# Performance work log

Measured on AMD Instinct MI355X. Metric: run time of the kernel, lower is better.

## Reference

```python
import jax, jax.numpy as jnp
import numpy as np

N_TIME, N_BATCH, N_STATE, N_FORCE = 64, 8192, 32, 16
DT = 0.05          # implicit (backward-Euler) step size
NEWTON_ITERS = 6   # fixed Newton-Raphson iteration count (converges well below fp32 eps here)


def setup_inputs() -> dict:
    key = jax.random.key(0)
    k = jax.random.split(key, 5)
    return {
        "y0": jax.random.normal(k[0], (N_BATCH, N_STATE), jnp.float32) * 0.1,
        "forces": jax.random.normal(k[1], (N_TIME, N_BATCH, N_FORCE), jnp.float32),
        "W": jax.random.normal(k[2], (N_STATE, N_STATE), jnp.float32) / np.float32(np.sqrt(N_STATE)),
        "U": jax.random.normal(k[3], (N_STATE, N_FORCE), jnp.float32) / np.float32(np.sqrt(N_FORCE)),
        "b": jax.random.normal(k[4], (N_STATE,), jnp.float32) * 0.01,
        "n": N_TIME,
    }


def reference(y0, forces, W, U, b, n):
    """Sequential recursive nonlinear solve, block_size=1, ZeroPredictor guess.

    Each step solves R(y_k) = y_k - y_{k-1} - dt*tanh(W y_k + U u_k + b) = 0
    via Newton-Raphson with a batched dense solve of the diagonal Jacobian
    block J[1] = I - dt*diag(1-t^2) W (the Thomas factorization for a single
    step reduces to this dense solve).
    """
    S = y0.shape[-1]
    I = jnp.eye(S, dtype=y0.dtype)

    def step(y_prev, u):
        fu = u @ U.T + b                      # [B,S] constant per Newton solve
        y = jnp.zeros_like(y_prev)            # ZeroPredictor initial guess
        for _ in range(NEWTON_ITERS):         # plain Newton-Raphson
            t = jnp.tanh(y @ W.T + fu)        # [B,S]
            R = y - y_prev - DT * t           # residual [B,S]
            J = I - DT * ((1.0 - t * t)[..., :, None] * W)  # [B,S,S] dR/dy
            y = y - jnp.linalg.solve(J, R[..., None])[..., 0]
        return y, y

    _, ys = jax.lax.scan(step, y0, forces[1:n])   # sequential recursion over time
    return jnp.concatenate([y0[None], ys], axis=0)  # result[0] = y0
```

## Files before the change

### kernel.cpp

```cpp
#include <hip/hip_runtime.h>

#define NT 64
#define NB 8192
#define NS 32
#define NF 16
#define DT 0.05f

typedef float f32x2 __attribute__((ext_vector_type(2)));
typedef float f32x4 __attribute__((ext_vector_type(4)));

__device__ __forceinline__ f32x2 tanh2(f32x2 x) {
    const float K = 2.8853900817779268f;
    float e0 = __builtin_amdgcn_exp2f(K * x[0]);
    float e1 = __builtin_amdgcn_exp2f(K * x[1]);
    float r0 = __builtin_amdgcn_rcpf(e0 + 1.0f);
    float r1 = __builtin_amdgcn_rcpf(e1 + 1.0f);
    f32x2 r;
    r[0] = fmaf(-2.0f, r0, 1.0f);
    r[1] = fmaf(-2.0f, r1, 1.0f);
    return r;
}

__global__ __launch_bounds__(256, 2) void rnes_kernel(
    const float* __restrict__ y0,
    const float* __restrict__ forces,
    const float* __restrict__ W,
    const float* __restrict__ U,
    const float* __restrict__ bias,
    float* __restrict__ out)
{
    const int lane = threadIdx.x & 63;
    const int wv   = threadIdx.x >> 6;
    const int b    = lane >> 4;
    const int p    = lane & 15;
    const int batch = blockIdx.x * 16 + wv * 4 + b;

    const int got = __builtin_amdgcn_update_dpp(0, p, 0x121, 0xF, 0xF, true) & 15;
    const int dir = (got == ((p + 1) & 15)) ? 1 : 15;

    f32x2 WA[16], WB[16];
#pragma unroll
    for (int j = 0; j < 16; ++j) {
        const int q = (p + dir * j) & 15;
        WA[j] = *(const f32x2*)(W + (2*p)   * NS + 2*q);
        WB[j] = *(const f32x2*)(W + (2*p+1) * NS + 2*q);
    }
#pragma unroll
    for (int j = 0; j < 16; ++j)
        asm volatile("" : "+v"(WA[j]), "+v"(WB[j]));

    f32x2 UA[8], UB[8];
#pragma unroll
    for (int f = 0; f < 8; ++f) {
        UA[f] = *(const f32x2*)(U + (2*p)   * NF + 2*f);
        UB[f] = *(const f32x2*)(U + (2*p+1) * NF + 2*f);
    }
#pragma unroll
    for (int f = 0; f < 8; ++f)
        asm volatile("" : "+v"(UA[f]), "+v"(UB[f]));

    const f32x2 b2 = *(const f32x2*)(bias + 2*p);

    f32x2 yp = *(const f32x2*)(y0 + (size_t)batch * NS + 2*p);
    __builtin_nontemporal_store(yp, (f32x2*)(out + (size_t)batch * NS + 2*p));
    f32x2 ypp = yp;

    const size_t fstep = (size_t)NB * NF;
    const f32x4* fb = (const f32x4*)(forces + (size_t)batch * NF);
    f32x4 upf[4];
#pragma unroll
    for (int j = 0; j < 4; ++j)
        upf[j] = __builtin_nontemporal_load(&fb[(fstep >> 2) + j]);

    for (int k = 1; k < NT; ++k) {
        f32x2 sA = (f32x2){0.f, 0.f}, sB = (f32x2){0.f, 0.f};
#pragma unroll
        for (int f = 0; f < 8; ++f) {
            f32x4 u4 = upf[f >> 1];
            f32x2 u2 = (f & 1) ? (f32x2){u4[2], u4[3]} : (f32x2){u4[0], u4[1]};
            sA = UA[f] * u2 + sA;
            sB = UB[f] * u2 + sB;
        }
        const float fu0 = b2[0] + sA[0] + sA[1];
        const float fu1 = b2[1] + sB[0] + sB[1];

        {
            int kn = (k + 1 < NT) ? (k + 1) : (NT - 1);
#pragma unroll
            for (int j = 0; j < 4; ++j)
                upf[j] = __builtin_nontemporal_load(&fb[(size_t)kn * (fstep >> 2) + j]);
        }

        f32x2 y;
        y[0] = yp[0] + (yp[0] - ypp[0]);
        y[1] = yp[1] + (yp[1] - ypp[1]);

        auto iterate = [&]() {
            const int y0i = __float_as_int(y[0]);
            const int y1i = __float_as_int(y[1]);
            f32x2 accA = (f32x2){fu0, 0.f};
            f32x2 accB = (f32x2){fu1, 0.f};
            accA = WA[0] * y + accA;
            accB = WB[0] * y + accB;
#define RNES_HOP(J)                                                            \
            {                                                                  \
                f32x2 yq;                                                      \
                yq[0] = __int_as_float(__builtin_amdgcn_update_dpp(            \
                    0, y0i, 0x120 + (J), 0xF, 0xF, true));                     \
                yq[1] = __int_as_float(__builtin_amdgcn_update_dpp(            \
                    0, y1i, 0x120 + (J), 0xF, 0xF, true));                     \
                accA = WA[J] * yq + accA;                                      \
                accB = WB[J] * yq + accB;                                      \
            }
            RNES_HOP(1)  RNES_HOP(2)  RNES_HOP(3)  RNES_HOP(4)
            RNES_HOP(5)  RNES_HOP(6)  RNES_HOP(7)  RNES_HOP(8)
            RNES_HOP(9)  RNES_HOP(10) RNES_HOP(11) RNES_HOP(12)
            RNES_HOP(13) RNES_HOP(14) RNES_HOP(15)
#undef RNES_HOP
            f32x2 zt;
            zt[0] = accA[0] + accA[1];
            zt[1] = accB[0] + accB[1];
            f32x2 t = tanh2(zt);
            y[0] = fmaf(DT, t[0], yp[0]);
            y[1] = fmaf(DT, t[1], yp[1]);
        };
        iterate();
        iterate();
        if (k == 1) iterate();

        ypp = yp;
        yp = y;
        __builtin_nontemporal_store(y, (f32x2*)(out + ((size_t)k * NB + batch) * NS + 2*p));
    }
}

extern "C" void kernel_launch(void* const* d_in, const int* in_sizes, int n_in,
                              void* d_out, int out_size, void* d_ws, size_t ws_size,
                              hipStream_t stream) {
    const float* y0     = (const float*)d_in[0];
    const float* forces = (const float*)d_in[1];
    const float* W      = (const float*)d_in[2];
    const float* U      = (const float*)d_in[3];
    const float* b      = (const float*)d_in[4];
    float* out = (float*)d_out;

    dim3 grid(NB / 16);
    dim3 block(256);
    rnes_kernel<<<grid, block, 0, stream>>>(y0, forces, W, U, b, out);
}
```

Before: 160.1 us.

## Split each batch row across two 16-lane halves to halve per-lane work

Each batch element now uses 32 lanes instead of 16. Each half-wave computes one of the two output rows per lane pair, and the halves exchange results through a ds_swizzle. This halves the per-lane FMA chain, W/U register footprint and tanh work, and raises the launch-bounds occupancy hint from 2 to 4. The cost is twice as many waves, redundant DPP traffic, an extra cross-lane swizzle per Newton iteration, and half the lanes idling on stores.

```diff
diff --git a/kernel.cpp b/kernel.cpp
--- a/kernel.cpp
+++ b/kernel.cpp
@@ -9,19 +9,18 @@
 typedef float f32x2 __attribute__((ext_vector_type(2)));
 typedef float f32x4 __attribute__((ext_vector_type(4)));
 
-__device__ __forceinline__ f32x2 tanh2(f32x2 x) {
+__device__ __forceinline__ float tanh1(float x) {
     const float K = 2.8853900817779268f;
-    float e0 = __builtin_amdgcn_exp2f(K * x[0]);
-    float e1 = __builtin_amdgcn_exp2f(K * x[1]);
-    float r0 = __builtin_amdgcn_rcpf(e0 + 1.0f);
-    float r1 = __builtin_amdgcn_rcpf(e1 + 1.0f);
-    f32x2 r;
-    r[0] = fmaf(-2.0f, r0, 1.0f);
-    r[1] = fmaf(-2.0f, r1, 1.0f);
-    return r;
+    float e = __builtin_amdgcn_exp2f(K * x);
+    float r = __builtin_amdgcn_rcpf(e + 1.0f);
+    return fmaf(-2.0f, r, 1.0f);
 }
 
-__global__ __launch_bounds__(256, 2) void rnes_kernel(
+__device__ __forceinline__ float swz16f(float v) {
+    return __int_as_float(__builtin_amdgcn_ds_swizzle(__float_as_int(v), 0x401F));
+}
+
+__global__ __launch_bounds__(256, 4) void rnes_kernel(
     const float* __restrict__ y0,
     const float* __restrict__ forces,
     const float* __restrict__ W,
@@ -31,38 +30,30 @@
 {
     const int lane = threadIdx.x & 63;
     const int wv   = threadIdx.x >> 6;
-    const int b    = lane >> 4;
+    const int b    = lane >> 5;
+    const int h    = (lane >> 4) & 1;
     const int p    = lane & 15;
-    const int batch = blockIdx.x * 16 + wv * 4 + b;
+    const int batch = blockIdx.x * 8 + wv * 2 + b;
+    const int o    = 2 * p + h;
 
     const int got = __builtin_amdgcn_update_dpp(0, p, 0x121, 0xF, 0xF, true) & 15;
     const int dir = (got == ((p + 1) & 15)) ? 1 : 15;
 
-    f32x2 WA[16], WB[16];
+    f32x2 W2[16];
 #pragma unroll
     for (int j = 0; j < 16; ++j) {
         const int q = (p + dir * j) & 15;
-        WA[j] = *(const f32x2*)(W + (2*p)   * NS + 2*q);
-        WB[j] = *(const f32x2*)(W + (2*p+1) * NS + 2*q);
+        W2[j] = *(const f32x2*)(W + o * NS + 2 * q);
     }
-#pragma unroll
-    for (int j = 0; j < 16; ++j)
-        asm volatile("" : "+v"(WA[j]), "+v"(WB[j]));
-
-    f32x2 UA[8], UB[8];
-#pragma unroll
-    for (int f = 0; f < 8; ++f) {
-        UA[f] = *(const f32x2*)(U + (2*p)   * NF + 2*f);
-        UB[f] = *(const f32x2*)(U + (2*p+1) * NF + 2*f);
-    }
+    f32x2 U2[8];
 #pragma unroll
     for (int f = 0; f < 8; ++f)
-        asm volatile("" : "+v"(UA[f]), "+v"(UB[f]));
+        U2[f] = *(const f32x2*)(U + o * NF + 2 * f);
+    const float bo = bias[o];
 
-    const f32x2 b2 = *(const f32x2*)(bias + 2*p);
-
-    f32x2 yp = *(const f32x2*)(y0 + (size_t)batch * NS + 2*p);
-    __builtin_nontemporal_store(yp, (f32x2*)(out + (size_t)batch * NS + 2*p));
+    f32x2 yp = *(const f32x2*)(y0 + (size_t)batch * NS + 2 * p);
+    if (h == 0)
+        __builtin_nontemporal_store(yp, (f32x2*)(out + (size_t)batch * NS + 2 * p));
     f32x2 ypp = yp;
 
     const size_t fstep = (size_t)NB * NF;
@@ -75,14 +66,14 @@
     for (int k = 1; k < NT; ++k) {
         f32x2 sA = (f32x2){0.f, 0.f}, sB = (f32x2){0.f, 0.f};
 #pragma unroll
-        for (int f = 0; f < 8; ++f) {
+        for (int f = 0; f < 8; f += 2) {
             f32x4 u4 = upf[f >> 1];
-            f32x2 u2 = (f & 1) ? (f32x2){u4[2], u4[3]} : (f32x2){u4[0], u4[1]};
-            sA = UA[f] * u2 + sA;
-            sB = UB[f] * u2 + sB;
+            f32x2 u20 = (f32x2){u4[0], u4[1]};
+            f32x2 u21 = (f32x2){u4[2], u4[3]};
+            sA = U2[f]     * u20 + sA;
+            sB = U2[f + 1] * u21 + sB;
         }
-        const float fu0 = b2[0] + sA[0] + sA[1];
-        const float fu1 = b2[1] + sB[0] + sB[1];
+        const float fu = bo + (sA[0] + sA[1]) + (sB[0] + sB[1]);
 
         {
             int kn = (k + 1 < NT) ? (k + 1) : (NT - 1);
@@ -91,6 +82,8 @@
                 upf[j] = __builtin_nontemporal_load(&fb[(size_t)kn * (fstep >> 2) + j]);
         }
 
+        const float ypo = h ? yp[1] : yp[0];
+
         f32x2 y;
         y[0] = yp[0] + (yp[0] - ypp[0]);
         y[1] = yp[1] + (yp[1] - ypp[1]);
@@ -98,10 +91,9 @@
         auto iterate = [&]() {
             const int y0i = __float_as_int(y[0]);
             const int y1i = __float_as_int(y[1]);
-            f32x2 accA = (f32x2){fu0, 0.f};
-            f32x2 accB = (f32x2){fu1, 0.f};
-            accA = WA[0] * y + accA;
-            accB = WB[0] * y + accB;
+            f32x2 acc0 = (f32x2){fu, 0.f};
+            f32x2 acc1 = (f32x2){0.f, 0.f};
+            acc0 = W2[0] * y + acc0;
 #define RNES_HOP(J)                                                            \
             {                                                                  \
                 f32x2 yq;                                                      \
@@ -109,20 +101,19 @@
                     0, y0i, 0x120 + (J), 0xF, 0xF, true));                     \
                 yq[1] = __int_as_float(__builtin_amdgcn_update_dpp(            \
                     0, y1i, 0x120 + (J), 0xF, 0xF, true));                     \
-                accA = WA[J] * yq + accA;                                      \
-                accB = WB[J] * yq + accB;                                      \
+                if ((J) & 1) acc1 = W2[J] * yq + acc1;                         \
+                else         acc0 = W2[J] * yq + acc0;                         \
             }
             RNES_HOP(1)  RNES_HOP(2)  RNES_HOP(3)  RNES_HOP(4)
             RNES_HOP(5)  RNES_HOP(6)  RNES_HOP(7)  RNES_HOP(8)
             RNES_HOP(9)  RNES_HOP(10) RNES_HOP(11) RNES_HOP(12)
             RNES_HOP(13) RNES_HOP(14) RNES_HOP(15)
 #undef RNES_HOP
-            f32x2 zt;
-            zt[0] = accA[0] + accA[1];
-            zt[1] = accB[0] + accB[1];
-            f32x2 t = tanh2(zt);
-            y[0] = fmaf(DT, t[0], yp[0]);
-            y[1] = fmaf(DT, t[1], yp[1]);
+            const float z = (acc0[0] + acc0[1]) + (acc1[0] + acc1[1]);
+            const float yn = fmaf(DT, tanh1(z), ypo);
+            const float yo = swz16f(yn);
+            y[0] = h ? yo : yn;
+            y[1] = h ? yn : yo;
         };
         iterate();
         iterate();
@@ -130,7 +121,8 @@
 
         ypp = yp;
         yp = y;
-        __builtin_nontemporal_store(y, (f32x2*)(out + ((size_t)k * NB + batch) * NS + 2*p));
+        if (h == 0)
+            __builtin_nontemporal_store(y, (f32x2*)(out + ((size_t)k * NB + batch) * NS + 2 * p));
     }
 }
 
@@ -144,7 +136,7 @@
     const float* b      = (const float*)d_in[4];
     float* out = (float*)d_out;
 
-    dim3 grid(NB / 16);
+    dim3 grid(NB / 8);
     dim3 block(256);
     rnes_kernel<<<grid, block, 0, stream>>>(y0, forces, W, U, b, out);
 }
```

After: 182.0 us. 13.7% more time.
